# Performance work log

Hardware: AMD Instinct MI355X
Metric: run time of the kernel (lower is better)

The kernel has to match this reference:

```python
import jax, jax.numpy as jnp
import numpy as np

K = 32
BN_EPS = 1e-5


def _fps(points, n_samples):
    # Sequential farthest point sampling; deterministic start at index 0
    # (torch version uses a random start; math otherwise identical).
    B, N, _ = points.shape

    def step(carry, _):
        dist_min, far = carry                                   # (B,N), (B,)
        c = jnp.take_along_axis(points, far[:, None, None].astype(jnp.int32) * jnp.ones((1, 1, 3), jnp.int32), axis=1)  # (B,1,3)
        d = jnp.sum((points - c) ** 2, axis=2)                  # (B,N)
        dist_min = jnp.minimum(dist_min, d)
        return (dist_min, jnp.argmax(dist_min, axis=1)), far

    init = (jnp.full((B, N), 1e10, points.dtype), jnp.zeros((B,), jnp.int64).astype(jnp.int32))
    _, cent = jax.lax.scan(step, init, None, length=n_samples)  # (n_samples, B)
    return cent.T                                               # (B, n_samples)


def _knn_idx(cntrds, pnts, k):
    # squared euclidean distance (same neighbor ordering as torch.cdist)
    d2 = (jnp.sum(cntrds ** 2, -1)[:, :, None]
          + jnp.sum(pnts ** 2, -1)[:, None, :]
          - 2.0 * jnp.einsum('bsc,bnc->bsn', cntrds, pnts))     # (B,ns,N)
    _, idx = jax.lax.top_k(-d2, k)                              # smallest-k
    return idx                                                  # (B,ns,k)


def _gather(x, idx):
    # x: (B,N,D), idx: (B,...) -> (B,...,D)
    return jax.vmap(lambda a, i: a[i])(x, idx)


def _conv1x1(x, w):
    # x: (B,Cin,ns,k), w: (Cout,Cin)
    return jnp.einsum('oc,bcnk->bonk', w, x)


def _bn_relu(x, g, b):
    # training-mode BatchNorm2d (biased variance over B,ns,k) + ReLU
    mean = jnp.mean(x, axis=(0, 2, 3), keepdims=True)
    var = jnp.var(x, axis=(0, 2, 3), keepdims=True)
    xh = (x - mean) * jax.lax.rsqrt(var + BN_EPS)
    return jax.nn.relu(xh * g[None, :, None, None] + b[None, :, None, None])


def setup_inputs() -> dict:
    key = jax.random.key(0)
    ks = jax.random.split(key, 16)
    B, N = 4, 4096
    s = 0.05
    return {
        'p': jax.random.normal(ks[0], (B, N, 3), jnp.float32),
        'f': jax.random.normal(ks[1], (B, 3, N), jnp.float32),
        'w1': jax.random.normal(ks[2], (256, 6), jnp.float32) * s,
        'w2': jax.random.normal(ks[3], (256, 256), jnp.float32) * s,
        'b2': jax.random.normal(ks[4], (256,), jnp.float32) * s,
        'g2': jnp.ones((256,), jnp.float32),
        'be2': jnp.zeros((256,), jnp.float32),
        'w3': jax.random.normal(ks[5], (512, 512), jnp.float32) * s,
        'g3': jnp.ones((512,), jnp.float32),
        'be3': jnp.zeros((512,), jnp.float32),
        'w4': jax.random.normal(ks[6], (256, 512), jnp.float32) * s,
        'g4': jnp.ones((256,), jnp.float32),
        'be4': jnp.zeros((256,), jnp.float32),
    }


def reference(p, f, w1, w2, b2, g2, be2, w3, g3, be3, w4, g4, be4):
    B, N, _ = p.shape
    ns = N // 4
    idx_c = _fps(p, ns)                                   # (B,ns)
    cntrd = _gather(p, idx_c)                             # (B,ns,3)
    feats = jnp.transpose(f, (0, 2, 1))                   # (B,N,3)
    knn = _knn_idx(cntrd, p, K)                           # (B,ns,K)
    dp = _gather(p, knn)                                  # (B,ns,K,3)
    fj = _gather(feats, knn)                              # (B,ns,K,3)
    x = jnp.transpose(jnp.concatenate([dp, fj], -1), (0, 3, 1, 2))  # (B,6,ns,K)
    # conv1: 6->256 (no bias), 256->256 (bias) + BN + ReLU
    x = _conv1x1(x, w1)
    x = _conv1x1(x, w2) + b2[None, :, None, None]
    x = _bn_relu(x, g2, be2)                              # (B,256,ns,K)
    xm = jnp.max(x, axis=-1, keepdims=True)
    x = jnp.concatenate([jnp.broadcast_to(xm, x.shape), x], axis=1)  # (B,512,ns,K)
    # conv2: 512->512 BN ReLU, 512->256 BN ReLU
    x = _bn_relu(_conv1x1(x, w3), g3, be3)
    x = _bn_relu(_conv1x1(x, w4), g4, be4)
    out_feat = jnp.max(x, axis=-1)                        # (B,256,ns)
    return cntrd, out_feat
```

## Files before the change

kernel.cpp:

```cpp
#include <hip/hip_runtime.h>
#include <hip/hip_bf16.h>

#define B_ 4
#define N_ 4096
#define NS_ 1024
#define KNN_ 32
#define NPOS_ 131072
#define BN_EPS_ 1e-5f

using bf16 = __hip_bfloat16;
typedef unsigned short us;
typedef __attribute__((ext_vector_type(8))) short short8;
typedef __attribute__((ext_vector_type(4))) float f32x4;
typedef unsigned long long ull;

__device__ __forceinline__ float bf2f(bf16 h){ return __bfloat162float(h); }
__device__ __forceinline__ us f2bfbits(float x){
    bf16 h = __float2bfloat16(x);
    return *reinterpret_cast<us*>(&h);
}
__device__ __forceinline__ float bits2f(us u){
    unsigned v = ((unsigned)u)<<16; return __uint_as_float(v);
}
__device__ __forceinline__ void unpack8(uint4 v, float* f){
    f[0]=__uint_as_float((v.x&0xFFFFu)<<16); f[1]=__uint_as_float(v.x&0xFFFF0000u);
    f[2]=__uint_as_float((v.y&0xFFFFu)<<16); f[3]=__uint_as_float(v.y&0xFFFF0000u);
    f[4]=__uint_as_float((v.z&0xFFFFu)<<16); f[5]=__uint_as_float(v.z&0xFFFF0000u);
    f[6]=__uint_as_float((v.w&0xFFFFu)<<16); f[7]=__uint_as_float(v.w&0xFFFF0000u);
}
__device__ __forceinline__ uint4 pack8(const float* f){
    uint4 v;
    v.x = (unsigned)f2bfbits(f[0]) | ((unsigned)f2bfbits(f[1])<<16);
    v.y = (unsigned)f2bfbits(f[2]) | ((unsigned)f2bfbits(f[3])<<16);
    v.z = (unsigned)f2bfbits(f[4]) | ((unsigned)f2bfbits(f[5])<<16);
    v.w = (unsigned)f2bfbits(f[6]) | ((unsigned)f2bfbits(f[7])<<16);
    return v;
}
__device__ __forceinline__ unsigned fmono(float v){
    unsigned u = __float_as_uint(v);
    return (u & 0x80000000u) ? ~u : (u | 0x80000000u);
}

template<int CTRL, int ROWM>
__device__ __forceinline__ float dppmaxf(float x){
    int xi = __float_as_int(x);
    int yi = __builtin_amdgcn_update_dpp(xi, xi, CTRL, ROWM, 0xF, false);
    return fmaxf(x, __int_as_float(yi));
}
template<int CTRL, int ROWM>
__device__ __forceinline__ float dppminf(float x){
    int xi = __float_as_int(x);
    int yi = __builtin_amdgcn_update_dpp(xi, xi, CTRL, ROWM, 0xF, false);
    return fminf(x, __int_as_float(yi));
}
__device__ __forceinline__ float wave_max_f32(float x){
    x = dppmaxf<0x111,0xF>(x);
    x = dppmaxf<0x112,0xF>(x);
    x = dppmaxf<0x114,0xF>(x);
    x = dppmaxf<0x118,0xF>(x);
    x = dppmaxf<0x142,0xA>(x);
    x = dppmaxf<0x143,0xC>(x);
    return __int_as_float(__builtin_amdgcn_readlane(__float_as_int(x), 63));
}
__device__ __forceinline__ float wave_min_f32(float x){
    x = dppminf<0x111,0xF>(x);
    x = dppminf<0x112,0xF>(x);
    x = dppminf<0x114,0xF>(x);
    x = dppminf<0x118,0xF>(x);
    x = dppminf<0x142,0xA>(x);
    x = dppminf<0x143,0xC>(x);
    return __int_as_float(__builtin_amdgcn_readlane(__float_as_int(x), 63));
}
__device__ __forceinline__ float rowsum16(float x){
    x += __int_as_float(__builtin_amdgcn_update_dpp(0, __float_as_int(x), 0x111, 0xF, 0xF, true));
    x += __int_as_float(__builtin_amdgcn_update_dpp(0, __float_as_int(x), 0x112, 0xF, 0xF, true));
    x += __int_as_float(__builtin_amdgcn_update_dpp(0, __float_as_int(x), 0x114, 0xF, 0xF, true));
    x += __int_as_float(__builtin_amdgcn_update_dpp(0, __float_as_int(x), 0x118, 0xF, 0xF, true));
    return x;
}
__device__ __forceinline__ float rowmax16(float x){
    x = dppmaxf<0x111,0xF>(x);
    x = dppmaxf<0x112,0xF>(x);
    x = dppmaxf<0x114,0xF>(x);
    x = dppmaxf<0x118,0xF>(x);
    return x;
}
__device__ __forceinline__ float rowmin16(float x){
    x = dppminf<0x111,0xF>(x);
    x = dppminf<0x112,0xF>(x);
    x = dppminf<0x114,0xF>(x);
    x = dppminf<0x118,0xF>(x);
    return x;
}
__device__ __forceinline__ float wave_sum_f32(float x){
    x = rowsum16(x);
    x += __int_as_float(__builtin_amdgcn_update_dpp(0, __float_as_int(x), 0x142, 0xA, 0xF, false));
    x += __int_as_float(__builtin_amdgcn_update_dpp(0, __float_as_int(x), 0x143, 0xC, 0xF, false));
    return __int_as_float(__builtin_amdgcn_readlane(__float_as_int(x), 63));
}
__device__ __forceinline__ float max16(const float* v){
    float a = fmaxf(fmaxf(fmaxf(v[0],v[1]),v[2]),v[3]);
    float b = fmaxf(fmaxf(fmaxf(v[4],v[5]),v[6]),v[7]);
    float c = fmaxf(fmaxf(fmaxf(v[8],v[9]),v[10]),v[11]);
    float d = fmaxf(fmaxf(fmaxf(v[12],v[13]),v[14]),v[15]);
    return fmaxf(fmaxf(a,b), fmaxf(c,d));
}
__device__ __forceinline__ float min16(const float* v){
    float a = fminf(fminf(fminf(v[0],v[1]),v[2]),v[3]);
    float b = fminf(fminf(fminf(v[4],v[5]),v[6]),v[7]);
    float c = fminf(fminf(fminf(v[8],v[9]),v[10]),v[11]);
    float d = fminf(fminf(fminf(v[12],v[13]),v[14]),v[15]);
    return fminf(fminf(a,b), fminf(c,d));
}

#define NSLOT 64

__global__ __launch_bounds__(256) void bn_coef(const float* __restrict__ part,
                                               const float* __restrict__ g,
                                               const float* __restrict__ be,
                                               int chbase, int C,
                                               float2* __restrict__ ab){
    int c = blockIdx.x*256 + threadIdx.x;
    if (c < C){
        const float* ps = part + (size_t)(chbase+c)*2*NSLOT;
        float s = 0.f, q = 0.f;
        #pragma unroll 8
        for (int i=0;i<NSLOT;i++){ s += ps[i]; q += ps[NSLOT+i]; }
        const float inv = 1.0f/(float)NPOS_;
        float mean = s*inv;
        float var  = q*inv - mean*mean;
        float a = g[c]*rsqrtf(var + BN_EPS_);
        ab[c] = make_float2(a, be[c] - mean*a);
    }
}

#define PXPAD 832
__global__ __launch_bounds__(256) void mega_kernel(const float* __restrict__ p,
                                                   const float* __restrict__ f,
                                                   float* __restrict__ cntrd,
                                                   float* __restrict__ part,
                                                   int* __restrict__ prog,
                                                   int* __restrict__ w26flag,
                                                   const float* __restrict__ w1,
                                                   const float* __restrict__ w2,
                                                   float* __restrict__ W26,
                                                   const float* __restrict__ b2,
                                                   const float* __restrict__ w3,
                                                   us* __restrict__ whi3,
                                                   const float* __restrict__ w4,
                                                   us* __restrict__ whi4,
                                                   bf16* __restrict__ z2,
                                                   unsigned* __restrict__ mxmn2){
    __shared__ float4 pxyz[N_ + PXPAD];
    __shared__ ull warr[2][4];
    __shared__ int knnS[32];
    __shared__ float Ws[6][256];
    __shared__ float xs[6][32];
    __shared__ int ciS;
    const int bid = blockIdx.x;
    const int t = threadIdx.x;
    const int lane = t & 63;
    const int wave = t >> 6;

    if (bid < 4){
        const int b = bid;
        const float* pb = p + (size_t)b*N_*3;
        float rx[16], ry[16], rz[16], dist[16];
        #pragma unroll
        for (int j=0;j<16;j++){
            int i = t*16+j;
            float x = pb[i*3+0];
            float y = pb[i*3+1];
            float z = pb[i*3+2];
            rx[j]=x; ry[j]=y; rz[j]=z;
            pxyz[i] = make_float4(x,y,z,0.f);
            dist[j]=1e10f;
        }
        __syncthreads();
        float4 c = pxyz[0];
        if (t==0){
            atomicExch(&prog[b*NS_], 1);
            cntrd[(size_t)(b*NS_)*3+0] = c.x;
            cntrd[(size_t)(b*NS_)*3+1] = c.y;
            cntrd[(size_t)(b*NS_)*3+2] = c.z;
        }
        for (int s=1; s<NS_; s++){
            #pragma unroll
            for (int j=0;j<16;j++){
                float dx = __fsub_rn(rx[j],c.x);
                float dy = __fsub_rn(ry[j],c.y);
                float dz = __fsub_rn(rz[j],c.z);
                float d  = __fadd_rn(__fadd_rn(__fmul_rn(dx,dx),__fmul_rn(dy,dy)),__fmul_rn(dz,dz));
                dist[j] = fminf(dist[j], d);
            }
            float lmax = max16(dist);
            float wmax = wave_max_f32(lmax);
            unsigned msk = 0;
            #pragma unroll
            for (int j=0;j<16;j++) msk |= (dist[j]==wmax) ? (1u<<j) : 0u;
            ull ball = __ballot(msk != 0);
            int srclane = (int)__builtin_ctzll(ball);
            unsigned lmsk = (unsigned)__builtin_amdgcn_readlane((int)msk, srclane);
            int widx = (wave*64 + srclane)*16 + (int)__builtin_ctz(lmsk);
            if (lane==0)
                warr[s&1][wave] = ((ull)__float_as_uint(wmax)<<32) | (0xFFFFFFFFu - (unsigned)widx);
            __syncthreads();
            ull g0 = warr[s&1][0], g1 = warr[s&1][1], g2 = warr[s&1][2], g3 = warr[s&1][3];
            ull ga = g0 > g1 ? g0 : g1;
            ull gb = g2 > g3 ? g2 : g3;
            ull g  = ga > gb ? ga : gb;
            int cur = (int)(0xFFFFFFFFu - (unsigned)(g & 0xFFFFFFFFull));
            c = pxyz[cur];
            if (t==0){
                atomicExch(&prog[b*NS_+s], cur+1);
                cntrd[(size_t)(b*NS_+s)*3+0] = c.x;
                cntrd[(size_t)(b*NS_+s)*3+1] = c.y;
                cntrd[(size_t)(b*NS_+s)*3+2] = c.z;
            }
        }
        return;
    }
    if (bid == 4){
        float acc[6] = {0,0,0,0,0,0};
        for (int k=0;k<256;k++){
            float w2v = w2[t*256+k];
            #pragma unroll
            for (int j=0;j<6;j++) acc[j] = fmaf(w2v, w1[k*6+j], acc[j]);
        }
        #pragma unroll
        for (int j=0;j<6;j++) W26[j*256+t] = acc[j];
        __syncthreads();
        if (t==0){ __threadfence(); atomicExch(w26flag, 1); }
        return;
    }
    if (bid < 1029){
        int i = (bid-5)*256 + t;
        whi3[i] = f2bfbits(w3[i]);
        return;
    }
    if (bid < 1541){
        int i = (bid-1029)*256 + t;
        whi4[i] = f2bfbits(w4[i]);
        return;
    }
    const int wid = bid - 1541;
    const int b = wid & 3;
    const int si = wid >> 2;
    const int sidx = b*NS_ + si;
    const float* pb = p + (size_t)b*N_*3;
    if (t == 0){
        int v;
        while ((v = atomicAdd(&prog[sidx], 0)) == 0) { __builtin_amdgcn_s_sleep(8); }
        ciS = v - 1;
    }
    __syncthreads();
    const int ci = ciS;
    float cx = pb[ci*3+0];
    float cy = pb[ci*3+1];
    float cz = pb[ci*3+2];
    float c2 = __fadd_rn(__fadd_rn(__fmul_rn(cx,cx),__fmul_rn(cy,cy)),__fmul_rn(cz,cz));
    float d2[16];
    #pragma unroll
    for (int j=0;j<16;j++){
        int i = t*16+j;
        float x = pb[i*3+0];
        float y = pb[i*3+1];
        float z = pb[i*3+2];
        float p2 = __fadd_rn(__fadd_rn(__fmul_rn(x,x),__fmul_rn(y,y)),__fmul_rn(z,z));
        float dot= __fadd_rn(__fadd_rn(__fmul_rn(cx,x),__fmul_rn(cy,y)),__fmul_rn(cz,z));
        d2[j] = __fsub_rn(__fadd_rn(c2,p2), __fmul_rn(2.0f,dot));
    }
    for (int it=0; it<KNN_; it++){
        float lmin = min16(d2);
        float wmin = wave_min_f32(lmin);
        unsigned msk = 0;
        #pragma unroll
        for (int j=0;j<16;j++) msk |= (d2[j]==wmin) ? (1u<<j) : 0u;
        ull ball = __ballot(msk != 0);
        int srclane = (int)__builtin_ctzll(ball);
        unsigned lmsk = (unsigned)__builtin_amdgcn_readlane((int)msk, srclane);
        int widx = (wave*64 + srclane)*16 + (int)__builtin_ctz(lmsk);
        if (lane==0)
            warr[it&1][wave] = ((ull)fmono(wmin)<<32) | (unsigned)widx;
        __syncthreads();
        ull g0 = warr[it&1][0], g1 = warr[it&1][1], g2 = warr[it&1][2], g3 = warr[it&1][3];
        ull ga = g0 < g1 ? g0 : g1;
        ull gb = g2 < g3 ? g2 : g3;
        ull g  = ga < gb ? ga : gb;
        int idx = (int)(g & 0xFFFFFFFFull);
        if ((idx>>4)==t) d2[idx & 15] = INFINITY;
        if (t==0) knnS[it] = idx;
    }
    if (t == 0){ while (atomicAdd(w26flag, 0) == 0) { __builtin_amdgcn_s_sleep(8); } __threadfence(); }
    __syncthreads();
    #pragma unroll
    for (int r=0;r<6;r++) Ws[r][t] = W26[r*256+t];
    if (t < 32){
        int i = knnS[t];
        const float* fb = f + (size_t)b*3*N_;
        xs[0][t] = pb[i*3+0];
        xs[1][t] = pb[i*3+1];
        xs[2][t] = pb[i*3+2];
        xs[3][t] = fb[0*N_+i];
        xs[4][t] = fb[1*N_+i];
        xs[5][t] = fb[2*N_+i];
    }
    __syncthreads();
    float w0=Ws[0][t], w1v=Ws[1][t], w2v=Ws[2][t], w3v=Ws[3][t], w4v=Ws[4][t], w5v=Ws[5][t];
    float bias = b2[t];
    bf16* zrow = z2 + (size_t)t*NPOS_ + (size_t)sidx*KNN_;
    float ssum = 0.f, sq = 0.f;
    float mxv = -3.4e38f, mnv = 3.4e38f;
    for (int k0=0;k0<32;k0+=8){
        float y[8];
        #pragma unroll
        for (int u=0;u<8;u++){
            int k = k0+u;
            float acc = bias;
            acc = fmaf(w0, xs[0][k], acc);
            acc = fmaf(w1v,xs[1][k], acc);
            acc = fmaf(w2v,xs[2][k], acc);
            acc = fmaf(w3v,xs[3][k], acc);
            acc = fmaf(w4v,xs[4][k], acc);
            acc = fmaf(w5v,xs[5][k], acc);
            float vr = bits2f(f2bfbits(acc));
            ssum += vr; sq = fmaf(vr, vr, sq);
            mxv = fmaxf(mxv, vr); mnv = fminf(mnv, vr);
            y[u] = acc;
        }
        *reinterpret_cast<uint4*>(zrow + k0) = pack8(y);
    }
    mxmn2[(size_t)sidx*256 + t] = (unsigned)f2bfbits(mxv) | ((unsigned)f2bfbits(mnv)<<16);
    const int slot = wid & (NSLOT-1);
    atomicAdd(&part[(size_t)(t*2+0)*NSLOT + slot], ssum);
    atomicAdd(&part[(size_t)(t*2+1)*NSLOT + slot], sq);
}

__global__ __launch_bounds__(256) void xm_kernel(const unsigned* __restrict__ mxmn2,
                                                 const float2* __restrict__ ab,
                                                 bf16* __restrict__ xm){
    const int t = threadIdx.x;
    const int bs0 = blockIdx.x * 32;
    float2 s = ab[t];
    us y[32];
    #pragma unroll
    for (int i=0;i<32;i++){
        unsigned v = mxmn2[(size_t)(bs0+i)*256 + t];
        float x = (s.x >= 0.f) ? bits2f((us)(v & 0xFFFFu)) : bits2f((us)(v >> 16));
        y[i] = f2bfbits(fmaxf(fmaf(x, s.x, s.y), 0.0f));
    }
    uint4* dst = reinterpret_cast<uint4*>(reinterpret_cast<us*>(xm) + (size_t)t*4096 + bs0);
    const uint4* src = reinterpret_cast<const uint4*>(y);
    dst[0]=src[0]; dst[1]=src[1]; dst[2]=src[2]; dst[3]=src[3];
}

__global__ __launch_bounds__(256) void gemm128(const float* __restrict__ A, int lda, int aoff,
                                               const bf16* __restrict__ B,
                                               int M, int N, int K,
                                               float* __restrict__ Cf){
    __shared__ float As[16][128];
    __shared__ float Bs[16][128];
    const int tid = threadIdx.x;
    const int tx = tid & 15, ty = tid >> 4;
    const int m0 = blockIdx.y*128, n0 = blockIdx.x*128;
    float acc[8][8];
    #pragma unroll
    for (int i=0;i<8;i++)
        #pragma unroll
        for (int j=0;j<8;j++) acc[i][j]=0.f;
    const int arow = tid >> 1, akg = tid & 1;
    const int bkk = tid >> 4, bng = tid & 15;
    for (int k0=0;k0<K;k0+=16){
        const float* aptr = A + (size_t)(m0+arow)*lda + aoff + k0 + akg*8;
        float4 a0 = *reinterpret_cast<const float4*>(aptr);
        float4 a1 = *reinterpret_cast<const float4*>(aptr+4);
        As[akg*8+0][arow]=a0.x; As[akg*8+1][arow]=a0.y;
        As[akg*8+2][arow]=a0.z; As[akg*8+3][arow]=a0.w;
        As[akg*8+4][arow]=a1.x; As[akg*8+5][arow]=a1.y;
        As[akg*8+6][arow]=a1.z; As[akg*8+7][arow]=a1.w;
        uint4 bv = *reinterpret_cast<const uint4*>(B + (size_t)(k0+bkk)*N + n0 + bng*8);
        float bf[8]; unpack8(bv, bf);
        *reinterpret_cast<float4*>(&Bs[bkk][bng*8+0]) = make_float4(bf[0],bf[1],bf[2],bf[3]);
        *reinterpret_cast<float4*>(&Bs[bkk][bng*8+4]) = make_float4(bf[4],bf[5],bf[6],bf[7]);
        __syncthreads();
        #pragma unroll
        for (int kk=0;kk<16;kk++){
            float a[8], b[8];
            *reinterpret_cast<float4*>(&a[0]) = *reinterpret_cast<float4*>(&As[kk][ty*8+0]);
            *reinterpret_cast<float4*>(&a[4]) = *reinterpret_cast<float4*>(&As[kk][ty*8+4]);
            *reinterpret_cast<float4*>(&b[0]) = *reinterpret_cast<float4*>(&Bs[kk][tx*8+0]);
            *reinterpret_cast<float4*>(&b[4]) = *reinterpret_cast<float4*>(&Bs[kk][tx*8+4]);
            #pragma unroll
            for (int i=0;i<8;i++)
                #pragma unroll
                for (int j=0;j<8;j++)
                    acc[i][j] = fmaf(a[i], b[j], acc[i][j]);
        }
        __syncthreads();
    }
    const int n = n0 + tx*8;
    #pragma unroll
    for (int i=0;i<8;i++){
        int m = m0 + ty*8 + i;
        *reinterpret_cast<float4*>(Cf + (size_t)m*N + n + 0) = make_float4(acc[i][0],acc[i][1],acc[i][2],acc[i][3]);
        *reinterpret_cast<float4*>(Cf + (size_t)m*N + n + 4) = make_float4(acc[i][4],acc[i][5],acc[i][6],acc[i][7]);
    }
}

#define LDK 40
__global__ __launch_bounds__(256) void gemm_mfma(const us* __restrict__ Whi,
                                                 int ldw, int aoff,
                                                 const bf16* __restrict__ act, int K,
                                                 const float2* __restrict__ ab,
                                                 bf16* __restrict__ out,
                                                 const float* __restrict__ t3,
                                                 float* __restrict__ part, int chbase,
                                                 unsigned* __restrict__ mxmnout){
    __shared__ __align__(16) us AsH[128*LDK];
    __shared__ __align__(16) us Bs [128*LDK];
    __shared__ float t3s[128][4];
    const us* actu = reinterpret_cast<const us*>(act);
    const int t = threadIdx.x;
    const int m0 = blockIdx.x*128, n0 = blockIdx.y*128;
    const int wave = t>>6, lane = t&63;
    const int wm = wave>>1, wn = wave&1;
    const int q = lane>>4, col = lane&15;

    if (t3 && t < 128){
        const float* src = t3 + (size_t)(m0+t)*4096 + (n0>>5);
        t3s[t][0]=src[0]; t3s[t][1]=src[1]; t3s[t][2]=src[2]; t3s[t][3]=src[3];
    }

    f32x4 acc[4][4];
    #pragma unroll
    for (int i=0;i<4;i++)
        #pragma unroll
        for (int j=0;j<4;j++) acc[i][j] = (f32x4){0.f,0.f,0.f,0.f};

    const int ar = t>>1, ah = t&1;
    const int bn = t&127, bh = t>>7;

    for (int k0=0;k0<K;k0+=32){
        const us* sh = Whi + (size_t)(m0+ar)*ldw + aoff + k0 + ah*16;
        uint4 h0 = *reinterpret_cast<const uint4*>(sh);
        uint4 h1 = *reinterpret_cast<const uint4*>(sh+8);
        *reinterpret_cast<uint4*>(&AsH[ar*LDK + ah*16 + 0]) = h0;
        *reinterpret_cast<uint4*>(&AsH[ar*LDK + ah*16 + 8]) = h1;
        us bvals[16];
        #pragma unroll
        for (int j=0;j<16;j++){
            int k = k0 + bh*16 + j;
            float x = bits2f(actu[(size_t)k*NPOS_ + n0 + bn]);
            float2 s = ab[k];
            bvals[j] = f2bfbits(fmaxf(fmaf(x, s.x, s.y), 0.0f));
        }
        *reinterpret_cast<uint4*>(&Bs[bn*LDK + bh*16 + 0]) = *reinterpret_cast<uint4*>(&bvals[0]);
        *reinterpret_cast<uint4*>(&Bs[bn*LDK + bh*16 + 8]) = *reinterpret_cast<uint4*>(&bvals[8]);
        __syncthreads();
        short8 bf[4], afh[4];
        #pragma unroll
        for (int tn=0;tn<4;tn++)
            bf[tn] = *reinterpret_cast<const short8*>(&Bs[(wn*64+tn*16+col)*LDK + q*8]);
        #pragma unroll
        for (int tm=0;tm<4;tm++)
            afh[tm] = *reinterpret_cast<const short8*>(&AsH[(wm*64+tm*16+col)*LDK + q*8]);
        #pragma unroll
        for (int tm=0;tm<4;tm++)
            #pragma unroll
            for (int tn=0;tn<4;tn++)
                acc[tm][tn] = __builtin_amdgcn_mfma_f32_16x16x32_bf16(afh[tm], bf[tn], acc[tm][tn], 0, 0, 0);
        __syncthreads();
    }
    const int slot = (int)(blockIdx.y & (NSLOT-1));
    #pragma unroll
    for (int tm=0;tm<4;tm++){
        #pragma unroll
        for (int r=0;r<4;r++){
            int m_l = wm*64 + tm*16 + q*4 + r;
            float srow = 0.f, qrow = 0.f;
            float vr4[4];
            #pragma unroll
            for (int tn=0;tn<4;tn++){
                int n_l = wn*64 + tn*16 + col;
                float vv = acc[tm][tn][r];
                if (t3) vv += t3s[m_l][n_l>>5];
                us hb = f2bfbits(vv);
                if (!mxmnout)
                    reinterpret_cast<us*>(out)[(size_t)(m0+m_l)*NPOS_ + n0 + n_l] = hb;
                float vr = bits2f(hb);
                vr4[tn] = vr;
                srow += vr; qrow = fmaf(vr, vr, qrow);
            }
            srow = rowsum16(srow);
            qrow = rowsum16(qrow);
            if (col == 15){
                atomicAdd(&part[(size_t)((chbase + m0 + m_l)*2+0)*NSLOT + slot], srow);
                atomicAdd(&part[(size_t)((chbase + m0 + m_l)*2+1)*NSLOT + slot], qrow);
            }
            if (mxmnout){
                unsigned pk[2];
                #pragma unroll
                for (int h=0;h<2;h++){
                    float mxl = fmaxf(vr4[2*h], vr4[2*h+1]);
                    float mnl = fminf(vr4[2*h], vr4[2*h+1]);
                    mxl = rowmax16(mxl);
                    mnl = rowmin16(mnl);
                    pk[h] = (unsigned)f2bfbits(mxl) | ((unsigned)f2bfbits(mnl)<<16);
                }
                if (col == 15){
                    int bsi = (n0>>5) + wn*2;
                    *reinterpret_cast<uint2*>(&mxmnout[(size_t)(m0+m_l)*4096 + bsi]) =
                        make_uint2(pk[0], pk[1]);
                }
            }
        }
    }
}

__global__ __launch_bounds__(256) void final_kernel(const unsigned* __restrict__ mxmn4,
                                                    const float* __restrict__ part,
                                                    const float* __restrict__ g4,
                                                    const float* __restrict__ be4,
                                                    float* __restrict__ out){
    __shared__ float abS[2];
    const int t = threadIdx.x;
    const int c = (blockIdx.x >> 2) & 255;
    const int b = blockIdx.x >> 10;
    const int s = ((blockIdx.x & 3) << 8) | t;
    if (t < 64){
        float ss = part[(size_t)((768+c)*2+0)*NSLOT + t];
        float qq = part[(size_t)((768+c)*2+1)*NSLOT + t];
        ss = wave_sum_f32(ss);
        qq = wave_sum_f32(qq);
        if (t==0){
            const float inv = 1.0f/(float)NPOS_;
            float mean = ss*inv;
            float var  = qq*inv - mean*mean;
            float a = g4[c]*rsqrtf(var + BN_EPS_);
            abS[0] = a; abS[1] = be4[c] - mean*a;
        }
    }
    __syncthreads();
    const float a = abS[0], bb = abS[1];
    const int bsi = b*NS_ + s;
    unsigned v = mxmn4[(size_t)c*4096 + bsi];
    float x = (a >= 0.f) ? bits2f((us)(v & 0xFFFFu)) : bits2f((us)(v >> 16));
    out[(size_t)(b*256 + c)*NS_ + s] = fmaxf(fmaf(x, a, bb), 0.0f);
}

extern "C" void kernel_launch(void* const* d_in, const int* in_sizes, int n_in,
                              void* d_out, int out_size, void* d_ws, size_t ws_size,
                              hipStream_t stream) {
    const float* p   = (const float*)d_in[0];
    const float* f   = (const float*)d_in[1];
    const float* w1  = (const float*)d_in[2];
    const float* w2  = (const float*)d_in[3];
    const float* b2  = (const float*)d_in[4];
    const float* g2  = (const float*)d_in[5];
    const float* be2 = (const float*)d_in[6];
    const float* w3  = (const float*)d_in[7];
    const float* g3  = (const float*)d_in[8];
    const float* be3 = (const float*)d_in[9];
    const float* w4  = (const float*)d_in[10];
    const float* g4  = (const float*)d_in[11];
    const float* be4 = (const float*)d_in[12];

    char* ws = (char*)d_ws;
    float*    W26   = (float*)(ws + 540672);
    float2*   ab2   = (float2*)(ws + 555008);
    float2*   ab3   = (float2*)(ws + 557056);
    us*       whi3  = (us*)(ws + 561152);
    us*       whi4  = (us*)(ws + 1609728);
    float*    t3    = (float*)(ws + 2134016);
    unsigned* mxmn2 = (unsigned*)(ws + 2134016);
    bf16*     z2    = (bf16*)(ws + 10522624);
    unsigned* mxmn4 = (unsigned*)(ws + 10522624);
    bf16*     xm    = (bf16*)(ws + 77631488);
    bf16*     z3    = (bf16*)(ws + 79728640);
    float*    part  = (float*)(ws + 213946368);
    int*      prog  = (int*)(ws + 214470656);
    int*      w26flag = (int*)(ws + 214487040);

    float* out_cntrd = (float*)d_out;
    float* out_feat  = (float*)d_out + (size_t)B_*NS_*3;

    hipMemsetAsync(ws + 213946368, 0, 540676, stream);
    mega_kernel<<<5637, 256, 0, stream>>>(p, f, out_cntrd, part, prog, w26flag,
                                          w1, w2, W26, b2,
                                          w3, whi3, w4, whi4, z2, mxmn2);
    bn_coef<<<1, 256, 0, stream>>>(part, g2, be2, 0, 256, ab2);
    xm_kernel<<<128, 256, 0, stream>>>(mxmn2, ab2, xm);
    gemm128<<<dim3(32,4), 256, 0, stream>>>(w3, 512, 0, xm, 512, 4096, 256, t3);
    gemm_mfma<<<dim3(4,1024), 256, 0, stream>>>(whi3, 512, 256, z2, 256, ab2, z3, t3, part, 256,
                                                nullptr);
    bn_coef<<<2, 256, 0, stream>>>(part, g3, be3, 256, 512, ab3);
    gemm_mfma<<<dim3(2,1024), 256, 0, stream>>>(whi4, 512, 0, z3, 512, ab3, nullptr, nullptr, part, 768,
                                                mxmn4);
    final_kernel<<<4096, 256, 0, stream>>>(mxmn4, part, g4, be4, out_feat);
}
```

Measured before the change: 1.066 ms.

## Process two batches per FPS block to halve sequential barrier overhead

```diff
diff --git a/kernel.cpp b/kernel.cpp
--- a/kernel.cpp
+++ b/kernel.cpp
@@ -134,7 +134,6 @@
     }
 }
 
-#define PXPAD 832
 __global__ __launch_bounds__(256) void mega_kernel(const float* __restrict__ p,
                                                    const float* __restrict__ f,
                                                    float* __restrict__ cntrd,
@@ -151,8 +150,8 @@
                                                    us* __restrict__ whi4,
                                                    bf16* __restrict__ z2,
                                                    unsigned* __restrict__ mxmn2){
-    __shared__ float4 pxyz[N_ + PXPAD];
-    __shared__ ull warr[2][4];
+    __shared__ float4 pxyz[2][N_];
+    __shared__ ull warr[2][4][2];
     __shared__ int knnS[32];
     __shared__ float Ws[6][256];
     __shared__ float xs[6][32];
@@ -162,65 +161,100 @@
     const int lane = t & 63;
     const int wave = t >> 6;
 
-    if (bid < 4){
-        const int b = bid;
-        const float* pb = p + (size_t)b*N_*3;
-        float rx[16], ry[16], rz[16], dist[16];
+    if (bid < 2){
+        const int b0 = bid*2, b1 = bid*2+1;
+        const float* pb0 = p + (size_t)b0*N_*3;
+        const float* pb1 = p + (size_t)b1*N_*3;
+        float rx0[16], ry0[16], rz0[16], dist0[16];
+        float rx1[16], ry1[16], rz1[16], dist1[16];
         #pragma unroll
         for (int j=0;j<16;j++){
             int i = t*16+j;
-            float x = pb[i*3+0];
-            float y = pb[i*3+1];
-            float z = pb[i*3+2];
-            rx[j]=x; ry[j]=y; rz[j]=z;
-            pxyz[i] = make_float4(x,y,z,0.f);
-            dist[j]=1e10f;
+            float x0 = pb0[i*3+0], y0 = pb0[i*3+1], z0 = pb0[i*3+2];
+            rx0[j]=x0; ry0[j]=y0; rz0[j]=z0;
+            pxyz[0][i] = make_float4(x0,y0,z0,0.f);
+            dist0[j]=1e10f;
+            float x1 = pb1[i*3+0], y1 = pb1[i*3+1], z1 = pb1[i*3+2];
+            rx1[j]=x1; ry1[j]=y1; rz1[j]=z1;
+            pxyz[1][i] = make_float4(x1,y1,z1,0.f);
+            dist1[j]=1e10f;
         }
         __syncthreads();
-        float4 c = pxyz[0];
+        float4 c0 = pxyz[0][0];
+        float4 c1 = pxyz[1][0];
         if (t==0){
-            atomicExch(&prog[b*NS_], 1);
-            cntrd[(size_t)(b*NS_)*3+0] = c.x;
-            cntrd[(size_t)(b*NS_)*3+1] = c.y;
-            cntrd[(size_t)(b*NS_)*3+2] = c.z;
+            atomicExch(&prog[b0*NS_], 1);
+            atomicExch(&prog[b1*NS_], 1);
+            cntrd[(size_t)(b0*NS_)*3+0] = c0.x;
+            cntrd[(size_t)(b0*NS_)*3+1] = c0.y;
+            cntrd[(size_t)(b0*NS_)*3+2] = c0.z;
+            cntrd[(size_t)(b1*NS_)*3+0] = c1.x;
+            cntrd[(size_t)(b1*NS_)*3+1] = c1.y;
+            cntrd[(size_t)(b1*NS_)*3+2] = c1.z;
         }
         for (int s=1; s<NS_; s++){
             #pragma unroll
             for (int j=0;j<16;j++){
-                float dx = __fsub_rn(rx[j],c.x);
-                float dy = __fsub_rn(ry[j],c.y);
-                float dz = __fsub_rn(rz[j],c.z);
-                float d  = __fadd_rn(__fadd_rn(__fmul_rn(dx,dx),__fmul_rn(dy,dy)),__fmul_rn(dz,dz));
-                dist[j] = fminf(dist[j], d);
+                float dx0 = __fsub_rn(rx0[j],c0.x);
+                float dy0 = __fsub_rn(ry0[j],c0.y);
+                float dz0 = __fsub_rn(rz0[j],c0.z);
+                float d0  = __fadd_rn(__fadd_rn(__fmul_rn(dx0,dx0),__fmul_rn(dy0,dy0)),__fmul_rn(dz0,dz0));
+                dist0[j] = fminf(dist0[j], d0);
+                float dx1 = __fsub_rn(rx1[j],c1.x);
+                float dy1 = __fsub_rn(ry1[j],c1.y);
+                float dz1 = __fsub_rn(rz1[j],c1.z);
+                float d1  = __fadd_rn(__fadd_rn(__fmul_rn(dx1,dx1),__fmul_rn(dy1,dy1)),__fmul_rn(dz1,dz1));
+                dist1[j] = fminf(dist1[j], d1);
             }
-            float lmax = max16(dist);
-            float wmax = wave_max_f32(lmax);
-            unsigned msk = 0;
+            float lmax0 = max16(dist0);
+            float lmax1 = max16(dist1);
+            float wmax0 = wave_max_f32(lmax0);
+            float wmax1 = wave_max_f32(lmax1);
+            unsigned msk0 = 0, msk1 = 0;
             #pragma unroll
-            for (int j=0;j<16;j++) msk |= (dist[j]==wmax) ? (1u<<j) : 0u;
-            ull ball = __ballot(msk != 0);
-            int srclane = (int)__builtin_ctzll(ball);
-            unsigned lmsk = (unsigned)__builtin_amdgcn_readlane((int)msk, srclane);
-            int widx = (wave*64 + srclane)*16 + (int)__builtin_ctz(lmsk);
-            if (lane==0)
-                warr[s&1][wave] = ((ull)__float_as_uint(wmax)<<32) | (0xFFFFFFFFu - (unsigned)widx);
+            for (int j=0;j<16;j++){
+                msk0 |= (dist0[j]==wmax0) ? (1u<<j) : 0u;
+                msk1 |= (dist1[j]==wmax1) ? (1u<<j) : 0u;
+            }
+            ull ball0 = __ballot(msk0 != 0);
+            ull ball1 = __ballot(msk1 != 0);
+            int sl0 = (int)__builtin_ctzll(ball0);
+            int sl1 = (int)__builtin_ctzll(ball1);
+            unsigned lm0 = (unsigned)__builtin_amdgcn_readlane((int)msk0, sl0);
+            unsigned lm1 = (unsigned)__builtin_amdgcn_readlane((int)msk1, sl1);
+            int wi0 = (wave*64 + sl0)*16 + (int)__builtin_ctz(lm0);
+            int wi1 = (wave*64 + sl1)*16 + (int)__builtin_ctz(lm1);
+            if (lane==0){
+                warr[s&1][wave][0] = ((ull)__float_as_uint(wmax0)<<32) | (0xFFFFFFFFu - (unsigned)wi0);
+                warr[s&1][wave][1] = ((ull)__float_as_uint(wmax1)<<32) | (0xFFFFFFFFu - (unsigned)wi1);
+            }
             __syncthreads();
-            ull g0 = warr[s&1][0], g1 = warr[s&1][1], g2 = warr[s&1][2], g3 = warr[s&1][3];
-            ull ga = g0 > g1 ? g0 : g1;
-            ull gb = g2 > g3 ? g2 : g3;
-            ull g  = ga > gb ? ga : gb;
-            int cur = (int)(0xFFFFFFFFu - (unsigned)(g & 0xFFFFFFFFull));
-            c = pxyz[cur];
+            ull a0 = warr[s&1][0][0], a1 = warr[s&1][1][0], a2 = warr[s&1][2][0], a3 = warr[s&1][3][0];
+            ull e0 = warr[s&1][0][1], e1 = warr[s&1][1][1], e2 = warr[s&1][2][1], e3 = warr[s&1][3][1];
+            ull ga0 = a0 > a1 ? a0 : a1;
+            ull gb0 = a2 > a3 ? a2 : a3;
+            ull g0  = ga0 > gb0 ? ga0 : gb0;
+            ull ga1 = e0 > e1 ? e0 : e1;
+            ull gb1 = e2 > e3 ? e2 : e3;
+            ull g1  = ga1 > gb1 ? ga1 : gb1;
+            int cur0 = (int)(0xFFFFFFFFu - (unsigned)(g0 & 0xFFFFFFFFull));
+            int cur1 = (int)(0xFFFFFFFFu - (unsigned)(g1 & 0xFFFFFFFFull));
+            c0 = pxyz[0][cur0];
+            c1 = pxyz[1][cur1];
             if (t==0){
-                atomicExch(&prog[b*NS_+s], cur+1);
-                cntrd[(size_t)(b*NS_+s)*3+0] = c.x;
-                cntrd[(size_t)(b*NS_+s)*3+1] = c.y;
-                cntrd[(size_t)(b*NS_+s)*3+2] = c.z;
+                atomicExch(&prog[b0*NS_+s], cur0+1);
+                atomicExch(&prog[b1*NS_+s], cur1+1);
+                cntrd[(size_t)(b0*NS_+s)*3+0] = c0.x;
+                cntrd[(size_t)(b0*NS_+s)*3+1] = c0.y;
+                cntrd[(size_t)(b0*NS_+s)*3+2] = c0.z;
+                cntrd[(size_t)(b1*NS_+s)*3+0] = c1.x;
+                cntrd[(size_t)(b1*NS_+s)*3+1] = c1.y;
+                cntrd[(size_t)(b1*NS_+s)*3+2] = c1.z;
             }
         }
         return;
     }
-    if (bid == 4){
+    if (bid == 2){
         float acc[6] = {0,0,0,0,0,0};
         for (int k=0;k<256;k++){
             float w2v = w2[t*256+k];
@@ -233,17 +267,17 @@
         if (t==0){ __threadfence(); atomicExch(w26flag, 1); }
         return;
     }
-    if (bid < 1029){
-        int i = (bid-5)*256 + t;
+    if (bid < 1027){
+        int i = (bid-3)*256 + t;
         whi3[i] = f2bfbits(w3[i]);
         return;
     }
-    if (bid < 1541){
-        int i = (bid-1029)*256 + t;
+    if (bid < 1539){
+        int i = (bid-1027)*256 + t;
         whi4[i] = f2bfbits(w4[i]);
         return;
     }
-    const int wid = bid - 1541;
+    const int wid = bid - 1539;
     const int b = wid & 3;
     const int si = wid >> 2;
     const int sidx = b*NS_ + si;
@@ -281,9 +315,9 @@
         unsigned lmsk = (unsigned)__builtin_amdgcn_readlane((int)msk, srclane);
         int widx = (wave*64 + srclane)*16 + (int)__builtin_ctz(lmsk);
         if (lane==0)
-            warr[it&1][wave] = ((ull)fmono(wmin)<<32) | (unsigned)widx;
+            warr[it&1][wave][0] = ((ull)fmono(wmin)<<32) | (unsigned)widx;
         __syncthreads();
-        ull g0 = warr[it&1][0], g1 = warr[it&1][1], g2 = warr[it&1][2], g3 = warr[it&1][3];
+        ull g0 = warr[it&1][0][0], g1 = warr[it&1][1][0], g2 = warr[it&1][2][0], g3 = warr[it&1][3][0];
         ull ga = g0 < g1 ? g0 : g1;
         ull gb = g2 < g3 ? g2 : g3;
         ull g  = ga < gb ? ga : gb;
@@ -585,7 +619,7 @@
     float* out_feat  = (float*)d_out + (size_t)B_*NS_*3;
 
     hipMemsetAsync(ws + 213946368, 0, 540676, stream);
-    mega_kernel<<<5637, 256, 0, stream>>>(p, f, out_cntrd, part, prog, w26flag,
+    mega_kernel<<<5635, 256, 0, stream>>>(p, f, out_cntrd, part, prog, w26flag,
                                           w1, w2, W26, b2,
                                           w3, whi3, w4, whi4, z2, mxmn2);
     bn_coef<<<1, 256, 0, stream>>>(part, g2, be2, 0, 256, ab2);
```

New measurement: 1.551 ms. 45.5% more time.
